# Optimization experiments

Hardware: AMD Instinct MI355X
Metric: run time of the kernel (lower is better)

The kernel has to match this reference:

```python
import jax, jax.numpy as jnp
import numpy as np

DIM = 1024
HID = 1536  # int(1024 * 1.5)
K = 4       # conv kernel size
N, T = 4, 4096


def _mk_forget_base(h, a=0.001, b=0.1, lo=-4.323, hi=-9.0):
    x = np.log(np.expm1(np.linspace(a, b, h, dtype=np.float64)))
    x = (x - x.min()) / (x.max() - x.min())
    x = x * abs(hi - lo) + hi
    return jnp.asarray(x, dtype=jnp.float32)


def setup_inputs() -> dict:
    key = jax.random.key(0)
    ks = jax.random.split(key, 6)
    x = jax.random.normal(ks[0], (N, T, DIM), jnp.float32)
    Wi = jax.random.normal(ks[1], (2 * HID, DIM), jnp.float32) * DIM ** -0.5
    conv_w = jax.random.normal(ks[2], (HID, 1, K), jnp.float32) * K ** -0.5
    conv_b = jax.random.normal(ks[3], (HID,), jnp.float32) * 0.01
    Wg = jax.random.normal(ks[4], (2 * HID, HID), jnp.float32) * HID ** -0.5
    bg = jnp.zeros((2 * HID,), jnp.float32)
    forget_base = _mk_forget_base(HID)
    Wo = jax.random.normal(ks[5], (DIM, HID), jnp.float32) * HID ** -0.5
    return {"x": x, "Wi": Wi, "conv_w": conv_w, "conv_b": conv_b,
            "Wg": Wg, "bg": bg, "forget_base": forget_base, "Wo": Wo}


def reference(x, Wi, conv_w, conv_b, Wg, bg, forget_base, Wo):
    # input projection -> gate, x  (each [N,T,HID])
    gi = jnp.einsum('ntc,hc->nth', x, Wi)
    gate, u = jnp.split(gi, 2, axis=-1)
    # causal depthwise conv1d (torch pads k-1 both sides then slices [:T])
    u = jax.lax.conv_general_dilated(
        u.transpose(0, 2, 1),            # [N,HID,T]
        conv_w,                           # [HID,1,K]
        window_strides=(1,),
        padding=[(K - 1, 0)],
        dimension_numbers=('NCH', 'OIH', 'NCH'),
        feature_group_count=HID,
    ) + conv_b[None, :, None]
    u = u.transpose(0, 2, 1)              # [N,T,HID]
    # gates
    fg = jnp.einsum('nth,gh->ntg', u, Wg) + bg
    forget, inp = jnp.split(fg, 2, axis=-1)
    # RG-LRU decay: alpha = exp(-8 * softplus(forget_base) * sigmoid(forget))
    alpha = jnp.exp(-8.0 * jax.nn.softplus(forget_base) * jax.nn.sigmoid(forget))
    beta = jnp.sqrt(1.0 - alpha ** 2 + 1e-6)
    xt = beta * jax.nn.sigmoid(inp) * u
    # linear recurrence h_t = alpha_t * h_{t-1} + x_t
    def step(h, ax):
        a, xx = ax
        h = a * h + xx
        return h, h
    _, h = jax.lax.scan(step, jnp.zeros((x.shape[0], HID), x.dtype),
                        (alpha.transpose(1, 0, 2), xt.transpose(1, 0, 2)))
    h = h.transpose(1, 0, 2)              # [N,T,HID]
    # output projection with exact (erf) gelu gate, matching torch default
    return jnp.einsum('nth,ch->ntc', jax.nn.gelu(gate, approximate=False) * h, Wo)
```

## Files before the change

### kernel.cpp

```cpp
#include <hip/hip_runtime.h>

#define DIM 1024
#define HID 1536
#define TT 4096
#define NB 4
#define KCONV 4
#define MROWS (NB * TT)
#define NC 256
#define CH (TT / NC)
#define H8 (HID / 8)
#define H4 (HID / 4)
#define TC 16

typedef unsigned short u16;
typedef short bf16x8 __attribute__((ext_vector_type(8)));
typedef u16 u16x4 __attribute__((ext_vector_type(4)));
typedef float f32x4 __attribute__((ext_vector_type(4)));

__device__ __forceinline__ u16 f2bf(float f) {
  union { float f; unsigned u; } v; v.f = f;
  unsigned r = (v.u + 0x7fffu + ((v.u >> 16) & 1u)) >> 16;
  return (u16)r;
}
__device__ __forceinline__ float bf2f(u16 h) {
  union { unsigned u; float f; } v; v.u = ((unsigned)h) << 16;
  return v.f;
}
__device__ __forceinline__ float gelu_exact(float g) {
  return 0.5f * g * (1.0f + erff(g * 0.70710678118f));
}

__global__ void cvt_all(const float* __restrict__ s0, u16* __restrict__ d0, int n0,
                        const float* __restrict__ s1, u16* __restrict__ d1, int n1,
                        const float* __restrict__ s2, u16* __restrict__ d2, int n2,
                        const float* __restrict__ s3, u16* __restrict__ d3, int n3) {
  int i = blockIdx.x * blockDim.x + threadIdx.x;
  const float* s; u16* d; int k;
  if (i < n0) { s = s0; d = d0; k = i; }
  else if (i < n0 + n1) { s = s1; d = d1; k = i - n0; }
  else if (i < n0 + n1 + n2) { s = s2; d = d2; k = i - n0 - n1; }
  else if (i < n0 + n1 + n2 + n3) { s = s3; d = d3; k = i - n0 - n1 - n2; }
  else return;
  float4 v = reinterpret_cast<const float4*>(s)[k];
  ushort4 o;
  o.x = f2bf(v.x); o.y = f2bf(v.y); o.z = f2bf(v.z); o.w = f2bf(v.w);
  reinterpret_cast<ushort4*>(d)[k] = o;
}

#define AS1q __attribute__((address_space(1)))
#define AS3q __attribute__((address_space(3)))
__device__ __forceinline__ void glds16(const u16* g, u16* l) {
  __builtin_amdgcn_global_load_lds((const AS1q void*)g, (AS3q void*)l, 16, 0, 0);
}

#define BAR    asm volatile("s_barrier" ::: "memory")
#define WAITV4 asm volatile("s_waitcnt vmcnt(4)" ::: "memory")
#define WAITV0 asm volatile("s_waitcnt vmcnt(0)" ::: "memory")
#define SCHED0 __builtin_amdgcn_sched_barrier(0)

template <int EPI>
__global__ __launch_bounds__(512, 2) void gemm256(
    const u16* __restrict__ A, const u16* __restrict__ B,
    float* __restrict__ C, u16* __restrict__ O0, u16* __restrict__ O1,
    int M, int Nn, int K, int gx) {
  __shared__ u16 LA[2][2][8192];
  __shared__ u16 LB[2][2][8192];
  const int tid = threadIdx.x;
  const int l = tid & 63;
  const int wid = tid >> 6;
  const int wr = wid >> 2;
  const int wc = wid & 3;

  const int bid = blockIdx.x;
  const int gm8 = (M >> 8) >> 3;
  const int xcd = bid & 7;
  const int idx = bid >> 3;
  const int mg  = idx / (4 * gx);
  const int rem = idx % (4 * gx);
  const int nn  = rem >> 2;
  const int mi  = rem & 3;
  const int tileM = (xcd * gm8 + mg * 4 + mi) * 256;
  const int tileN = nn * 256;

  const int lp = l ^ ((l & 32) >> 4);
  const int srow = lp >> 2;
  const int scol = (lp & 3) * 8;
  const int rdoff = ((l & 15) * 32 + (l >> 4) * 8) ^ ((l & 8) << 1);

  const u16* Abase = A + (size_t)(tileM + wid * 32 + srow) * K + scol;
  const u16* Bbase = B + (size_t)(tileN + wid * 32 + srow) * K + scol;

#define STAGE_A(c, kk, kt) { const u16* g_ = Abase + (size_t)(kt) * 64 + (kk) * 32; \
    glds16(g_, &LA[c][kk][wid * 1024]); glds16(g_ + 16 * (size_t)K, &LA[c][kk][wid * 1024 + 512]); }
#define STAGE_B(c, kk, kt) { const u16* g_ = Bbase + (size_t)(kt) * 64 + (kk) * 32; \
    glds16(g_, &LB[c][kk][wid * 1024]); glds16(g_ + 16 * (size_t)K, &LB[c][kk][wid * 1024 + 512]); }

  f32x4 acc[8][4] = {};
  bf16x8 a[8], b[4];

#define LDB4(c, kk) { _Pragma("unroll") for (int ni = 0; ni < 4; ni++) \
    b[ni] = *(const bf16x8*)&LB[c][kk][(wc * 4 + ni) * 512 + rdoff]; }
#define LDA8(c, kk) { _Pragma("unroll") for (int mi2 = 0; mi2 < 8; mi2++) \
    a[mi2] = *(const bf16x8*)&LA[c][kk][(wr * 8 + mi2) * 512 + rdoff]; }
#define MFMA32 { __builtin_amdgcn_s_setprio(1); \
    _Pragma("unroll") for (int mi2 = 0; mi2 < 8; mi2++) \
    _Pragma("unroll") for (int ni = 0; ni < 4; ni++) \
      acc[mi2][ni] = __builtin_amdgcn_mfma_f32_16x16x32_bf16(a[mi2], b[ni], acc[mi2][ni], 0, 0, 0); \
    __builtin_amdgcn_s_setprio(0); }

  STAGE_A(0, 0, 0); STAGE_B(0, 0, 0);
  STAGE_A(0, 1, 0); STAGE_B(0, 1, 0);
  STAGE_A(1, 0, 1); STAGE_B(1, 0, 1);
  WAITV4; BAR;

  const int NIT = K >> 7;
  for (int i = 0; i < NIT; i++) {
    const int kt = 2 * i;
    const bool nl = (i + 1 < NIT);
    LDB4(0, 0); LDA8(0, 0); STAGE_A(1, 1, kt + 1); STAGE_B(1, 1, kt + 1);
    SCHED0; MFMA32; BAR;
    LDB4(0, 1); LDA8(0, 1); if (nl) { STAGE_A(0, 0, kt + 2); STAGE_B(0, 0, kt + 2); }
    SCHED0; MFMA32; if (nl) { WAITV4; } else { WAITV0; } BAR;
    LDB4(1, 0); LDA8(1, 0); if (nl) { STAGE_A(0, 1, kt + 2); STAGE_B(0, 1, kt + 2); }
    SCHED0; MFMA32; BAR;
    LDB4(1, 1); LDA8(1, 1); if (nl) { STAGE_A(1, 0, kt + 3); STAGE_B(1, 0, kt + 3); }
    SCHED0; MFMA32; if (nl) { WAITV4; } else { WAITV0; } BAR;
  }

  const int r0 = tileM + wr * 128 + (l >> 4) * 4;
  const int c0 = tileN + wc * 64 + (l & 15);
  if (EPI == 0) {
#pragma unroll
    for (int ai = 0; ai < 8; ai++)
#pragma unroll
      for (int ni = 0; ni < 4; ni++)
#pragma unroll
        for (int r = 0; r < 4; r++)
          C[(size_t)(r0 + ai * 16 + r) * Nn + (c0 + ni * 16)] = acc[ai][ni][r];
  } else {
    const bool lo = (tileN < HID);
    u16* dst = lo ? O0 : O1;
    const int cb = lo ? 0 : HID;
#pragma unroll
    for (int ai = 0; ai < 8; ai++)
#pragma unroll
      for (int ni = 0; ni < 4; ni++)
#pragma unroll
        for (int r = 0; r < 4; r++) {
          float v = acc[ai][ni][r];
          if (EPI == 2 && lo) v = gelu_exact(v);
          dst[(size_t)(r0 + ai * 16 + r) * HID + (c0 + ni * 16 - cb)] = f2bf(v);
        }
  }
#undef STAGE_A
#undef STAGE_B
#undef LDB4
#undef LDA8
#undef MFMA32
}

__global__ void conv1d_k(const u16* __restrict__ u, const float* __restrict__ w,
                         const float* __restrict__ b, u16* __restrict__ uc) {
  int idx = blockIdx.x * blockDim.x + threadIdx.x;
  int hb = (idx % H8) * 8;
  int rc = idx / H8;
  int t0 = (rc % (TT / TC)) * TC;
  int n  = rc / (TT / TC);

  float wt[KCONV][8], bias[8];
#pragma unroll
  for (int j = 0; j < 8; j++) {
    float4 wj = reinterpret_cast<const float4*>(w)[hb + j];
    wt[0][j] = wj.x; wt[1][j] = wj.y; wt[2][j] = wj.z; wt[3][j] = wj.w;
    bias[j] = b[hb + j];
  }

  const u16* up = u + (size_t)n * TT * HID + hb;
  u16* op = uc + (size_t)n * TT * HID + hb;
  bf16x8 zero;
#pragma unroll
  for (int j = 0; j < 8; j++) zero[j] = 0;
  bf16x8 w0 = (t0 > 0) ? *(const bf16x8*)&up[(size_t)(t0 - 3) * HID] : zero;
  bf16x8 w1 = (t0 > 0) ? *(const bf16x8*)&up[(size_t)(t0 - 2) * HID] : zero;
  bf16x8 w2 = (t0 > 0) ? *(const bf16x8*)&up[(size_t)(t0 - 1) * HID] : zero;
#pragma unroll 4
  for (int t = t0; t < t0 + TC; t++) {
    bf16x8 cur = *(const bf16x8*)&up[(size_t)t * HID];
    bf16x8 o;
#pragma unroll
    for (int j = 0; j < 8; j++) {
      float a = bias[j];
      a += bf2f((u16)w0[j]) * wt[0][j];
      a += bf2f((u16)w1[j]) * wt[1][j];
      a += bf2f((u16)w2[j]) * wt[2][j];
      a += bf2f((u16)cur[j]) * wt[3][j];
      o[j] = (short)f2bf(a);
    }
    *(bf16x8*)&op[(size_t)t * HID] = o;
    w0 = w1; w1 = w2; w2 = cur;
  }
}

__global__ void scan_phase1(const u16* __restrict__ fbuf, const u16* __restrict__ ibuf,
                            const u16* __restrict__ ubuf, const float* __restrict__ fb,
                            const float* __restrict__ bg,
                            float* __restrict__ Ac, float* __restrict__ Bc) {
  int tid = blockIdx.x * blockDim.x + threadIdx.x;
  int hb = (tid % H4) * 4;
  int nc = tid / H4;
  int n = nc % NB;
  int c = nc / NB;
  f32x4 fbv = *reinterpret_cast<const f32x4*>(&fb[hb]);
  f32x4 bgf = *reinterpret_cast<const f32x4*>(&bg[hb]);
  f32x4 bgi = *reinterpret_cast<const f32x4*>(&bg[HID + hb]);
  float c8[4], ap[4] = {1.f, 1.f, 1.f, 1.f}, hl[4] = {0.f, 0.f, 0.f, 0.f};
#pragma unroll
  for (int j = 0; j < 4; j++) c8[j] = 8.0f * log1pf(expf(fbv[j]));
  size_t base = ((size_t)n * TT + (size_t)c * CH) * HID + hb;
  for (int t = 0; t < CH; t++) {
    size_t ix = base + (size_t)t * HID;
    u16x4 f4 = *reinterpret_cast<const u16x4*>(&fbuf[ix]);
    u16x4 i4 = *reinterpret_cast<const u16x4*>(&ibuf[ix]);
    u16x4 u4 = *reinterpret_cast<const u16x4*>(&ubuf[ix]);
#pragma unroll
    for (int j = 0; j < 4; j++) {
      float f = bf2f(f4[j]) + bgf[j];
      float sf = 1.0f / (1.0f + expf(-f));
      float al = expf(-c8[j] * sf);
      float be = sqrtf(1.0f - al * al + 1e-6f);
      float xi = bf2f(i4[j]) + bgi[j];
      float si = 1.0f / (1.0f + expf(-xi));
      float xt = be * si * bf2f(u4[j]);
      hl[j] = al * hl[j] + xt;
      ap[j] *= al;
    }
  }
  size_t ci = ((size_t)c * NB + n) * HID + hb;
  *reinterpret_cast<f32x4*>(&Ac[ci]) = f32x4{ap[0], ap[1], ap[2], ap[3]};
  *reinterpret_cast<f32x4*>(&Bc[ci]) = f32x4{hl[0], hl[1], hl[2], hl[3]};
}

__global__ void scan_phase2(const float* __restrict__ Ac, const float* __restrict__ Bc,
                            float* __restrict__ Carry) {
  int tid = blockIdx.x * blockDim.x + threadIdx.x;
  int h = tid % HID;
  int n = tid / HID;
  float carry = 0.f;
#pragma unroll 4
  for (int c = 0; c < NC; c++) {
    size_t ci = ((size_t)c * NB + n) * HID + h;
    Carry[ci] = carry;
    carry = Ac[ci] * carry + Bc[ci];
  }
}

__global__ void scan_phase3(const u16* __restrict__ fbuf, const u16* __restrict__ ibuf,
                            const u16* __restrict__ ubuf, const u16* __restrict__ gbuf,
                            const float* __restrict__ fb, const float* __restrict__ bg,
                            const float* __restrict__ Carry, u16* __restrict__ gh) {
  int tid = blockIdx.x * blockDim.x + threadIdx.x;
  int hb = (tid % H4) * 4;
  int nc = tid / H4;
  int n = nc % NB;
  int c = nc / NB;
  f32x4 fbv = *reinterpret_cast<const f32x4*>(&fb[hb]);
  f32x4 bgf = *reinterpret_cast<const f32x4*>(&bg[hb]);
  f32x4 bgi = *reinterpret_cast<const f32x4*>(&bg[HID + hb]);
  float c8[4], hc[4];
#pragma unroll
  for (int j = 0; j < 4; j++) c8[j] = 8.0f * log1pf(expf(fbv[j]));
  size_t ci = ((size_t)c * NB + n) * HID + hb;
  f32x4 cv = *reinterpret_cast<const f32x4*>(&Carry[ci]);
#pragma unroll
  for (int j = 0; j < 4; j++) hc[j] = cv[j];
  size_t base = ((size_t)n * TT + (size_t)c * CH) * HID + hb;
  for (int t = 0; t < CH; t++) {
    size_t ix = base + (size_t)t * HID;
    u16x4 f4 = *reinterpret_cast<const u16x4*>(&fbuf[ix]);
    u16x4 i4 = *reinterpret_cast<const u16x4*>(&ibuf[ix]);
    u16x4 u4 = *reinterpret_cast<const u16x4*>(&ubuf[ix]);
    u16x4 g4 = *reinterpret_cast<const u16x4*>(&gbuf[ix]);
    u16x4 o4;
#pragma unroll
    for (int j = 0; j < 4; j++) {
      float f = bf2f(f4[j]) + bgf[j];
      float sf = 1.0f / (1.0f + expf(-f));
      float al = expf(-c8[j] * sf);
      float be = sqrtf(1.0f - al * al + 1e-6f);
      float xi = bf2f(i4[j]) + bgi[j];
      float si = 1.0f / (1.0f + expf(-xi));
      float xt = be * si * bf2f(u4[j]);
      hc[j] = al * hc[j] + xt;
      o4[j] = f2bf(bf2f(g4[j]) * hc[j]);
    }
    *reinterpret_cast<u16x4*>(&gh[ix]) = o4;
  }
}

extern "C" void kernel_launch(void* const* d_in, const int* in_sizes, int n_in,
                              void* d_out, int out_size, void* d_ws, size_t ws_size,
                              hipStream_t stream) {
  const float* x  = (const float*)d_in[0];
  const float* Wi = (const float*)d_in[1];
  const float* cw = (const float*)d_in[2];
  const float* cb = (const float*)d_in[3];
  const float* Wg = (const float*)d_in[4];
  const float* bg = (const float*)d_in[5];
  const float* fb = (const float*)d_in[6];
  const float* Wo = (const float*)d_in[7];
  float* out = (float*)d_out;

  const size_t SZ_XBF = (size_t)MROWS * DIM * 2;
  const size_t SZ_WI  = (size_t)2 * HID * DIM * 2;
  const size_t SZ_WG  = (size_t)2 * HID * HID * 2;
  const size_t SZ_WO  = (size_t)DIM * HID * 2;
  const size_t SZ_ACT = (size_t)MROWS * HID * 2;
  const size_t REQUIRED = SZ_XBF + SZ_WI + SZ_WG + SZ_WO + 4 * SZ_ACT;
  if (ws_size < REQUIRED) return;

  char* p = (char*)d_ws;
  auto alloc = [&](size_t bytes) { char* q = p; p += bytes; return q; };
  u16* x_bf   = (u16*)alloc(SZ_XBF);
  u16* Wi_bf  = (u16*)alloc(SZ_WI);
  u16* Wg_bf  = (u16*)alloc(SZ_WG);
  u16* Wo_bf  = (u16*)alloc(SZ_WO);
  u16* u_bf   = (u16*)alloc(SZ_ACT);
  u16* uc_bf  = (u16*)alloc(SZ_ACT);
  u16* fg0_bf = (u16*)alloc(SZ_ACT);
  u16* fg1_bf = (u16*)alloc(SZ_ACT);
  u16* gh_bf  = u_bf;

  u16* gate_bf = (u16*)d_out;
  float* Ac    = (float*)((char*)d_out + SZ_ACT);
  float* Bc    = Ac + (size_t)NC * NB * HID;
  float* Carry = Ac;

  const int n0 = MROWS * DIM / 4, n1 = 2 * HID * DIM / 4,
            n2 = 2 * HID * HID / 4, n3 = DIM * HID / 4;
  cvt_all<<<(n0 + n1 + n2 + n3 + 255) / 256, 256, 0, stream>>>(
      x, x_bf, n0, Wi, Wi_bf, n1, Wg, Wg_bf, n2, Wo, Wo_bf, n3);

  gemm256<2><<<(2 * HID / 256) * (MROWS / 256), 512, 0, stream>>>(
      x_bf, Wi_bf, nullptr, gate_bf, u_bf, MROWS, 2 * HID, DIM, 2 * HID / 256);
  conv1d_k<<<(NB * (TT / TC) * H8) / 256, 256, 0, stream>>>(u_bf, cw, cb, uc_bf);
  gemm256<1><<<(2 * HID / 256) * (MROWS / 256), 512, 0, stream>>>(
      uc_bf, Wg_bf, nullptr, fg0_bf, fg1_bf, MROWS, 2 * HID, HID, 2 * HID / 256);
  scan_phase1<<<(NB * H4 * NC) / 256, 256, 0, stream>>>(fg0_bf, fg1_bf, uc_bf, fb, bg, Ac, Bc);
  scan_phase2<<<(NB * HID) / 128, 128, 0, stream>>>(Ac, Bc, Carry);
  scan_phase3<<<(NB * H4 * NC) / 256, 256, 0, stream>>>(fg0_bf, fg1_bf, uc_bf, gate_bf, fb, bg, Carry, gh_bf);
  gemm256<0><<<(DIM / 256) * (MROWS / 256), 512, 0, stream>>>(
      gh_bf, Wo_bf, out, nullptr, nullptr, MROWS, DIM, HID, DIM / 256);
}
```

Baseline: 575.9 us.

## Use 16 waves per GEMM block with smaller per-wave tiles

After: 685.6 us. 19.0% more time.

```diff
diff --git a/kernel.cpp b/kernel.cpp
--- a/kernel.cpp
+++ b/kernel.cpp
@@ -55,11 +55,12 @@
 
 #define BAR    asm volatile("s_barrier" ::: "memory")
 #define WAITV4 asm volatile("s_waitcnt vmcnt(4)" ::: "memory")
+#define WAITV2 asm volatile("s_waitcnt vmcnt(2)" ::: "memory")
 #define WAITV0 asm volatile("s_waitcnt vmcnt(0)" ::: "memory")
 #define SCHED0 __builtin_amdgcn_sched_barrier(0)
 
 template <int EPI>
-__global__ __launch_bounds__(512, 2) void gemm256(
+__global__ __launch_bounds__(1024) void gemm256(
     const u16* __restrict__ A, const u16* __restrict__ B,
     float* __restrict__ C, u16* __restrict__ O0, u16* __restrict__ O1,
     int M, int Nn, int K, int gx) {
@@ -87,23 +88,21 @@
   const int scol = (lp & 3) * 8;
   const int rdoff = ((l & 15) * 32 + (l >> 4) * 8) ^ ((l & 8) << 1);
 
-  const u16* Abase = A + (size_t)(tileM + wid * 32 + srow) * K + scol;
-  const u16* Bbase = B + (size_t)(tileN + wid * 32 + srow) * K + scol;
-
-#define STAGE_A(c, kk, kt) { const u16* g_ = Abase + (size_t)(kt) * 64 + (kk) * 32; \
-    glds16(g_, &LA[c][kk][wid * 1024]); glds16(g_ + 16 * (size_t)K, &LA[c][kk][wid * 1024 + 512]); }
-#define STAGE_B(c, kk, kt) { const u16* g_ = Bbase + (size_t)(kt) * 64 + (kk) * 32; \
-    glds16(g_, &LB[c][kk][wid * 1024]); glds16(g_ + 16 * (size_t)K, &LB[c][kk][wid * 1024 + 512]); }
-
-  f32x4 acc[8][4] = {};
-  bf16x8 a[8], b[4];
+  const u16* Abase = A + (size_t)(tileM + wid * 16 + srow) * K + scol;
+  const u16* Bbase = B + (size_t)(tileN + wid * 16 + srow) * K + scol;
+
+#define STAGE_A(c, kk, kt) glds16(Abase + (size_t)(kt) * 64 + (kk) * 32, &LA[c][kk][wid * 512])
+#define STAGE_B(c, kk, kt) glds16(Bbase + (size_t)(kt) * 64 + (kk) * 32, &LB[c][kk][wid * 512])
+
+  f32x4 acc[4][4] = {};
+  bf16x8 a[4], b[4];
 
 #define LDB4(c, kk) { _Pragma("unroll") for (int ni = 0; ni < 4; ni++) \
     b[ni] = *(const bf16x8*)&LB[c][kk][(wc * 4 + ni) * 512 + rdoff]; }
-#define LDA8(c, kk) { _Pragma("unroll") for (int mi2 = 0; mi2 < 8; mi2++) \
-    a[mi2] = *(const bf16x8*)&LA[c][kk][(wr * 8 + mi2) * 512 + rdoff]; }
-#define MFMA32 { __builtin_amdgcn_s_setprio(1); \
-    _Pragma("unroll") for (int mi2 = 0; mi2 < 8; mi2++) \
+#define LDA4(c, kk) { _Pragma("unroll") for (int mi2 = 0; mi2 < 4; mi2++) \
+    a[mi2] = *(const bf16x8*)&LA[c][kk][(wr * 4 + mi2) * 512 + rdoff]; }
+#define MFMA16 { __builtin_amdgcn_s_setprio(1); \
+    _Pragma("unroll") for (int mi2 = 0; mi2 < 4; mi2++) \
     _Pragma("unroll") for (int ni = 0; ni < 4; ni++) \
       acc[mi2][ni] = __builtin_amdgcn_mfma_f32_16x16x32_bf16(a[mi2], b[ni], acc[mi2][ni], 0, 0, 0); \
     __builtin_amdgcn_s_setprio(0); }
@@ -117,21 +116,21 @@
   for (int i = 0; i < NIT; i++) {
     const int kt = 2 * i;
     const bool nl = (i + 1 < NIT);
-    LDB4(0, 0); LDA8(0, 0); STAGE_A(1, 1, kt + 1); STAGE_B(1, 1, kt + 1);
-    SCHED0; MFMA32; BAR;
-    LDB4(0, 1); LDA8(0, 1); if (nl) { STAGE_A(0, 0, kt + 2); STAGE_B(0, 0, kt + 2); }
-    SCHED0; MFMA32; if (nl) { WAITV4; } else { WAITV0; } BAR;
-    LDB4(1, 0); LDA8(1, 0); if (nl) { STAGE_A(0, 1, kt + 2); STAGE_B(0, 1, kt + 2); }
-    SCHED0; MFMA32; BAR;
-    LDB4(1, 1); LDA8(1, 1); if (nl) { STAGE_A(1, 0, kt + 3); STAGE_B(1, 0, kt + 3); }
-    SCHED0; MFMA32; if (nl) { WAITV4; } else { WAITV0; } BAR;
-  }
-
-  const int r0 = tileM + wr * 128 + (l >> 4) * 4;
+    LDB4(0, 0); LDA4(0, 0); STAGE_A(1, 1, kt + 1); STAGE_B(1, 1, kt + 1);
+    SCHED0; MFMA16; WAITV4; BAR;
+    LDB4(0, 1); LDA4(0, 1); if (nl) { STAGE_A(0, 0, kt + 2); STAGE_B(0, 0, kt + 2); }
+    SCHED0; MFMA16; if (nl) { WAITV4; } else { WAITV2; } BAR;
+    LDB4(1, 0); LDA4(1, 0); if (nl) { STAGE_A(0, 1, kt + 2); STAGE_B(0, 1, kt + 2); }
+    SCHED0; MFMA16; if (nl) { WAITV4; } else { WAITV0; } BAR;
+    LDB4(1, 1); LDA4(1, 1); if (nl) { STAGE_A(1, 0, kt + 3); STAGE_B(1, 0, kt + 3); }
+    SCHED0; MFMA16; if (nl) { WAITV4; } BAR;
+  }
+
+  const int r0 = tileM + wr * 64 + (l >> 4) * 4;
   const int c0 = tileN + wc * 64 + (l & 15);
   if (EPI == 0) {
 #pragma unroll
-    for (int ai = 0; ai < 8; ai++)
+    for (int ai = 0; ai < 4; ai++)
 #pragma unroll
       for (int ni = 0; ni < 4; ni++)
 #pragma unroll
@@ -142,7 +141,7 @@
     u16* dst = lo ? O0 : O1;
     const int cb = lo ? 0 : HID;
 #pragma unroll
-    for (int ai = 0; ai < 8; ai++)
+    for (int ai = 0; ai < 4; ai++)
 #pragma unroll
       for (int ni = 0; ni < 4; ni++)
 #pragma unroll
@@ -155,8 +154,8 @@
 #undef STAGE_A
 #undef STAGE_B
 #undef LDB4
-#undef LDA8
-#undef MFMA32
+#undef LDA4
+#undef MFMA16
 }
 
 __global__ void conv1d_k(const u16* __restrict__ u, const float* __restrict__ w,
@@ -340,14 +339,14 @@
   cvt_all<<<(n0 + n1 + n2 + n3 + 255) / 256, 256, 0, stream>>>(
       x, x_bf, n0, Wi, Wi_bf, n1, Wg, Wg_bf, n2, Wo, Wo_bf, n3);
 
-  gemm256<2><<<(2 * HID / 256) * (MROWS / 256), 512, 0, stream>>>(
+  gemm256<2><<<(2 * HID / 256) * (MROWS / 256), 1024, 0, stream>>>(
       x_bf, Wi_bf, nullptr, gate_bf, u_bf, MROWS, 2 * HID, DIM, 2 * HID / 256);
   conv1d_k<<<(NB * (TT / TC) * H8) / 256, 256, 0, stream>>>(u_bf, cw, cb, uc_bf);
-  gemm256<1><<<(2 * HID / 256) * (MROWS / 256), 512, 0, stream>>>(
+  gemm256<1><<<(2 * HID / 256) * (MROWS / 256), 1024, 0, stream>>>(
       uc_bf, Wg_bf, nullptr, fg0_bf, fg1_bf, MROWS, 2 * HID, HID, 2 * HID / 256);
   scan_phase1<<<(NB * H4 * NC) / 256, 256, 0, stream>>>(fg0_bf, fg1_bf, uc_bf, fb, bg, Ac, Bc);
   scan_phase2<<<(NB * HID) / 128, 128, 0, stream>>>(Ac, Bc, Carry);
   scan_phase3<<<(NB * H4 * NC) / 256, 256, 0, stream>>>(fg0_bf, fg1_bf, uc_bf, gate_bf, fb, bg, Carry, gh_bf);
-  gemm256<0><<<(DIM / 256) * (MROWS / 256), 512, 0, stream>>>(
+  gemm256<0><<<(DIM / 256) * (MROWS / 256), 1024, 0, stream>>>(
       gh_bf, Wo_bf, out, nullptr, nullptr, MROWS, DIM, HID, DIM / 256);
 }
```
